# Performance work log

Hardware: AMD Instinct MI355X
Metric: run time of the kernel (lower is better)

Reference implementation:

```python
import jax, jax.numpy as jnp
import numpy as np

D_EMBED = 2048
N_HEAD = 16
HEAD_DIM = D_EMBED // N_HEAD
B, S = 4, 2048


def setup_inputs() -> dict:
    key = jax.random.key(0)
    ks = jax.random.split(key, 6)
    s = 0.02
    x = jax.random.normal(ks[0], (B, S, D_EMBED), dtype=jnp.float32)
    attention_mask = jnp.ones((B, S), dtype=bool)
    Wq = jax.random.normal(ks[1], (D_EMBED, D_EMBED), dtype=jnp.float32) * s
    Wk = jax.random.normal(ks[2], (D_EMBED, D_EMBED), dtype=jnp.float32) * s
    Wv = jax.random.normal(ks[3], (D_EMBED, D_EMBED), dtype=jnp.float32) * s
    Wo = jax.random.normal(ks[4], (D_EMBED, D_EMBED), dtype=jnp.float32) * s
    bq = jnp.zeros((D_EMBED,), jnp.float32)
    bk = jnp.zeros((D_EMBED,), jnp.float32)
    bv = jnp.zeros((D_EMBED,), jnp.float32)
    bo = jnp.zeros((D_EMBED,), jnp.float32)
    return {"x": x, "attention_mask": attention_mask,
            "Wq": Wq, "bq": bq, "Wk": Wk, "bk": bk,
            "Wv": Wv, "bv": bv, "Wo": Wo, "bo": bo}


def reference(x, attention_mask, Wq, bq, Wk, bk, Wv, bv, Wo, bo):
    bsz, seq_len, _ = x.shape

    def split_heads(t):  # [B,S,D] -> [B,H,S,hd]
        return t.reshape(bsz, seq_len, N_HEAD, HEAD_DIM).transpose(0, 2, 1, 3)

    q = split_heads(x @ Wq + bq)
    k = split_heads(x @ Wk + bk)
    v = split_heads(x @ Wv + bv)

    scale = 1.0 / np.sqrt(HEAD_DIM).astype(np.float32)
    scores = jnp.einsum('bhqd,bhkd->bhqk', q, k) * scale  # [B,H,S,S]

    # causal (past_len = 0, query_len = total_len = S) combined with key padding mask
    causal = jnp.tril(jnp.ones((seq_len, seq_len), dtype=bool))  # [S,S]
    mask = causal[None, None, :, :] & attention_mask[:, None, None, :]
    neg = jnp.finfo(scores.dtype).min
    scores = jnp.where(mask, scores, neg)

    att = jax.nn.softmax(scores, axis=-1)  # dropout p=0.0 -> identity
    out = jnp.einsum('bhqk,bhkd->bhqd', att, v)
    out = out.transpose(0, 2, 1, 3).reshape(bsz, seq_len, D_EMBED)
    return out @ Wo + bo
```

## Files before the change

### kernel.cpp

```cpp
#include <hip/hip_runtime.h>
#include <cstdint>
#include <cstddef>


#define D_EMBED 2048
#define NHEAD   16
#define HDIM    128
#define BATCH   4
#define SEQ     2048
#define MROWS   (BATCH*SEQ)

typedef __attribute__((ext_vector_type(8))) short bf16x8;
typedef __attribute__((ext_vector_type(4))) float f32x4;

__device__ __forceinline__ short f2bf(float f) {
  union { float f; uint32_t u; } v; v.f = f;
  uint32_t r = v.u + 0x7fffu + ((v.u >> 16) & 1u);
  return (short)(r >> 16);
}

__device__ __forceinline__ void async_copy16(void* lds, const void* gmem) {
  __builtin_amdgcn_global_load_lds(
      (__attribute__((address_space(1))) void*)gmem,
      (__attribute__((address_space(3))) void*)lds, 16, 0, 0);
}

__global__ __launch_bounds__(256) void cvt_x(const float* __restrict__ x,
                                             short* __restrict__ xb) {
  int i = blockIdx.x * 256 + threadIdx.x;
  float4 v = reinterpret_cast<const float4*>(x)[i];
  short4 o;
  o.x = f2bf(v.x); o.y = f2bf(v.y); o.z = f2bf(v.z); o.w = f2bf(v.w);
  reinterpret_cast<short4*>(xb)[i] = o;
}

struct TransArgs { const float* src[4]; short* dst[4]; };

__global__ __launch_bounds__(256) void transpose_w(TransArgs ta) {
  const int z = blockIdx.z;
  const float* W = ta.src[z];
  short* Wt = ta.dst[z];
  __shared__ float tile[32][33];
  int bx = blockIdx.x * 32, by = blockIdx.y * 32;
  int tx = threadIdx.x & 31, ty = threadIdx.x >> 5;
#pragma unroll
  for (int r = ty; r < 32; r += 8)
    tile[r][tx] = W[(size_t)(by + r) * D_EMBED + bx + tx];
  __syncthreads();
#pragma unroll
  for (int r = ty; r < 32; r += 8)
    Wt[(size_t)(bx + r) * D_EMBED + by + tx] = f2bf(tile[tx][r]);
}

struct GemmArgs {
  const short* A;
  const short* Bt[3];
  const float* bias[3];
  void*        out[3];
  float        scale[3];
  int          mode[3];
};

__global__ __launch_bounds__(512, 2) void gemm256(GemmArgs ga) {
  const int z = blockIdx.z;
  const short* __restrict__ A  = ga.A;
  const short* __restrict__ Bt = ga.Bt[z];

  const int lin  = blockIdx.y * 8 + blockIdx.x;
  const int wg   = (lin & 7) * 32 + (lin >> 3);
  const int col0 = (wg & 7) * 256;
  const int row0 = (wg >> 3) * 256;

  __shared__ __align__(16) short As[2][2][2][64 * 64];
  __shared__ __align__(16) short Bs[2][2][128 * 64];

  const int tid  = threadIdx.x;
  const int lane = tid & 63, w = tid >> 6;
  const int lr   = lane & 15, quad = lane >> 4;
  const int wm   = w >> 2, wn = w & 3;
  const int lr8  = lane >> 3;
  const int srccol = ((lane & 7) ^ ((lane >> 3) & 7)) * 8;
  const int csw = (quad ^ (lr & 7)) * 8;

  bf16x8 av[4][2], bva[2][2], bvb[2][2];
  f32x4 acc[8][4] = {};

#define STAGE_A(buf, Mh, kk) do {                                              \
    _Pragma("unroll")                                                          \
    for (int j = 0; j < 2; ++j)                                                \
      async_copy16(&As[buf][Mh][j][w * 512],                                   \
          A + (size_t)(row0 + j * 128 + (Mh) * 64 + w * 8 + lr8) * D_EMBED +   \
              (kk) + srccol);                                                  \
  } while (0)

#define STAGE_B(buf, Nh, kk) do {                                              \
    _Pragma("unroll")                                                          \
    for (int j = 0; j < 2; ++j) {                                              \
      int fr_ = j * 64 + w * 8 + lr8;                                          \
      async_copy16(&Bs[buf][Nh][(j * 64 + w * 8) * 64],                        \
          Bt + (size_t)(col0 + (fr_ >> 5) * 64 + (Nh) * 32 + (fr_ & 31)) *     \
                  D_EMBED + (kk) + srccol);                                    \
    }                                                                          \
  } while (0)

#define LOAD_A(buf, Mh) do {                                                   \
    _Pragma("unroll")                                                          \
    for (int t = 0; t < 4; ++t) {                                              \
      const short* ap_ = &As[buf][Mh][wm][(t * 16 + lr) * 64];                 \
      av[t][0] = *reinterpret_cast<const bf16x8*>(ap_ + csw);                  \
      av[t][1] = *reinterpret_cast<const bf16x8*>(ap_ + (csw ^ 32));           \
    }                                                                          \
  } while (0)

#define LOAD_B(buf, Nh, dst) do {                                              \
    _Pragma("unroll")                                                          \
    for (int u = 0; u < 2; ++u) {                                              \
      const short* bp_ = &Bs[buf][Nh][(wn * 32 + u * 16 + lr) * 64];           \
      dst[u][0] = *reinterpret_cast<const bf16x8*>(bp_ + csw);                 \
      dst[u][1] = *reinterpret_cast<const bf16x8*>(bp_ + (csw ^ 32));          \
    }                                                                          \
  } while (0)

#define MFMA_Q(Mh, Nh, bv) do {                                                \
    _Pragma("unroll")                                                          \
    for (int ks = 0; ks < 2; ++ks)                                             \
      _Pragma("unroll")                                                        \
      for (int t = 0; t < 4; ++t)                                              \
        _Pragma("unroll")                                                      \
        for (int u = 0; u < 2; ++u)                                            \
          acc[(Mh) * 4 + t][(Nh) * 2 + u] =                                    \
              __builtin_amdgcn_mfma_f32_16x16x32_bf16(                         \
                  av[t][ks], bv[u][ks], acc[(Mh) * 4 + t][(Nh) * 2 + u],       \
                  0, 0, 0);                                                    \
  } while (0)

#define PHASE(Mh, Nh, bv) do {                                                 \
    __builtin_amdgcn_s_setprio(1);                                             \
    MFMA_Q(Mh, Nh, bv);                                                        \
    __builtin_amdgcn_s_setprio(0);                                             \
    __builtin_amdgcn_s_barrier();                                              \
  } while (0)

  STAGE_A(0, 0, 0);  STAGE_B(0, 0, 0);  STAGE_B(0, 1, 0);  STAGE_A(0, 1, 0);
  STAGE_A(1, 0, 64); STAGE_B(1, 0, 64); STAGE_B(1, 1, 64); STAGE_A(1, 1, 64);
  asm volatile("s_waitcnt vmcnt(0)" ::: "memory");
  __builtin_amdgcn_s_barrier();
  LOAD_B(0, 0, bva);

#pragma unroll 1
  for (int it = 0; it < 16; ++it) {
    const int kc = it * 128;
    LOAD_A(0, 0); LOAD_B(0, 1, bvb);
    PHASE(0, 0, bva);
    STAGE_A(0, 0, kc + 128); STAGE_B(0, 0, kc + 128);
    PHASE(0, 1, bvb);
    LOAD_A(0, 1);
    STAGE_B(0, 1, kc + 128);
    PHASE(1, 1, bvb);
    LOAD_B(1, 0, bvb);
    STAGE_A(0, 1, kc + 128);
    asm volatile("s_waitcnt vmcnt(4)" ::: "memory");
    PHASE(1, 0, bva);
    LOAD_A(1, 0); LOAD_B(1, 1, bva);
    PHASE(0, 0, bvb);
    STAGE_B(1, 0, kc + 192); STAGE_A(1, 0, kc + 192);
    PHASE(0, 1, bva);
    LOAD_A(1, 1);
    STAGE_B(1, 1, kc + 192);
    PHASE(1, 1, bva);
    LOAD_B(0, 0, bva);
    STAGE_A(1, 1, kc + 192);
    asm volatile("s_waitcnt vmcnt(4)" ::: "memory");
    PHASE(1, 0, bvb);
  }
  asm volatile("s_waitcnt vmcnt(0)" ::: "memory");

#undef STAGE_A
#undef STAGE_B
#undef LOAD_A
#undef LOAD_B
#undef MFMA_Q
#undef PHASE

  const float* __restrict__ bias = ga.bias[z];
  const int mode = ga.mode[z];
  const float scl = ga.scale[z];
  if (mode != 2) {
#pragma unroll
    for (int mi = 0; mi < 8; ++mi)
#pragma unroll
      for (int ni = 0; ni < 4; ++ni) {
        int n = col0 + wn * 64 + ni * 16 + lr;
        float bias_n = bias[n];
#pragma unroll
        for (int i = 0; i < 4; ++i) {
          int m = row0 + wm * 128 + mi * 16 + quad * 4 + i;
          float v = (acc[mi][ni][i] + bias_n) * scl;
          if (mode == 0) ((short*)ga.out[z])[(size_t)m * D_EMBED + n] = f2bf(v);
          else           ((float*)ga.out[z])[(size_t)m * D_EMBED + n] = v;
        }
      }
  } else {
    short* Vt = (short*)ga.out[z];
#pragma unroll
    for (int ni = 0; ni < 4; ++ni) {
      int n = col0 + wn * 64 + ni * 16 + lr;
      int h = n >> 7, dd = n & (HDIM - 1);
      float bias_n = bias[n];
#pragma unroll
      for (int mi = 0; mi < 8; ++mi)
#pragma unroll
        for (int i = 0; i < 4; ++i) {
          int m = row0 + wm * 128 + mi * 16 + quad * 4 + i;
          int b = m >> 11, t = m & (SEQ - 1);
          Vt[(size_t)((b * NHEAD + h) * HDIM + dd) * SEQ + t] = f2bf(acc[mi][ni][i] + bias_n);
        }
    }
  }
}

#define QK_ONE(Kp, qf, sc)                                                      \
  {                                                                             \
    _Pragma("unroll")                                                           \
    for (int nt = 0; nt < 4; ++nt) sc[nt] = (f32x4){0.f, 0.f, 0.f, 0.f};        \
    __builtin_amdgcn_s_setprio(1);                                              \
    _Pragma("unroll")                                                           \
    for (int nt = 0; nt < 4; ++nt)                                              \
      _Pragma("unroll")                                                         \
      for (int ks = 0; ks < 4; ++ks) {                                          \
        bf16x8 kf = *reinterpret_cast<const bf16x8*>(                           \
            &(Kp)[(nt * 16 + lr) * 128 + (((ks * 4 + quad) ^ lr) * 8)]);        \
        sc[nt] = __builtin_amdgcn_mfma_f32_16x16x32_bf16(qf[ks], kf, sc[nt], 0, 0, 0); \
      }                                                                         \
    __builtin_amdgcn_s_setprio(0);                                              \
  }

#define SM_ONE(sc, l_i, qrow, diag, t0)                                         \
  {                                                                             \
    if (diag) {                                                                 \
      _Pragma("unroll")                                                         \
      for (int nt = 0; nt < 4; ++nt) {                                          \
        int t = (t0) + nt * 16 + lr;                                            \
        _Pragma("unroll")                                                       \
        for (int i = 0; i < 4; ++i)                                             \
          if (t > (qrow) + quad * 4 + i) sc[nt][i] = -1e30f;                    \
      }                                                                         \
    }                                                                           \
    _Pragma("unroll")                                                           \
    for (int nt = 0; nt < 4; ++nt)                                              \
      _Pragma("unroll")                                                         \
      for (int i = 0; i < 4; ++i) {                                             \
        float p = exp2f(sc[nt][i]);                                             \
        l_i[i] += p;                                                            \
        Pls[wave][(quad * 4 + i) * 72 + nt * 16 + lr] = f2bf(p);                \
      }                                                                         \
  }

#define PV_ONE(Vp, o)                                                           \
  {                                                                             \
    __builtin_amdgcn_s_setprio(1);                                              \
    _Pragma("unroll")                                                           \
    for (int n2 = 0; n2 < 8; ++n2)                                              \
      _Pragma("unroll")                                                         \
      for (int k2 = 0; k2 < 2; ++k2) {                                          \
        bf16x8 pf = *reinterpret_cast<const bf16x8*>(                           \
            &Pls[wave][lr * 72 + k2 * 32 + quad * 8]);                          \
        bf16x8 vf = *reinterpret_cast<const bf16x8*>(                           \
            &(Vp)[(n2 * 16 + lr) * 64 + (((k2 * 4 + quad) ^ (lr & 7)) * 8)]);   \
        o[n2] = __builtin_amdgcn_mfma_f32_16x16x32_bf16(pf, vf, o[n2], 0, 0, 0);\
      }                                                                         \
    __builtin_amdgcn_s_setprio(0);                                              \
  }

#define FINALIZE_STRIP(o, l_i, qrow)                                            \
  {                                                                             \
    _Pragma("unroll")                                                           \
    for (int off = 1; off < 16; off <<= 1)                                      \
      _Pragma("unroll")                                                         \
      for (int i = 0; i < 4; ++i) l_i[i] += __shfl_xor(l_i[i], off);            \
    float inv_l[4];                                                             \
    _Pragma("unroll")                                                           \
    for (int i = 0; i < 4; ++i) inv_l[i] = 1.0f / l_i[i];                       \
    short* obase = O + (size_t)(b * SEQ + (qrow)) * D_EMBED + h * HDIM;         \
    _Pragma("unroll")                                                           \
    for (int n2 = 0; n2 < 8; ++n2)                                              \
      _Pragma("unroll")                                                         \
      for (int i = 0; i < 4; ++i)                                               \
        obase[(size_t)(quad * 4 + i) * D_EMBED + n2 * 16 + lr] =                \
            f2bf(o[n2][i] * inv_l[i]);                                          \
  }

#define STAGE_K(cb, tbase)                                                      \
  {                                                                             \
    _Pragma("unroll")                                                           \
    for (int s = 0; s < 4; ++s) {                                               \
      int r0 = wave * 16 + s * 4;                                               \
      int r  = r0 + krow;                                                       \
      int cg = (kcg_base ^ ((s * 4 + krow) & 15)) * 8;                          \
      async_copy16(&Kls[cb][r0 * 128],                                          \
                   Kbase + (size_t)((tbase) + r) * D_EMBED + cg);               \
    }                                                                           \
  }

#define STAGE_V(cb, tbase)                                                      \
  {                                                                             \
    _Pragma("unroll")                                                           \
    for (int s = 0; s < 4; ++s) {                                               \
      int r0 = wave * 32 + s * 8;                                               \
      int r  = r0 + vrow;                                                       \
      async_copy16(&Vls[cb][r0 * 64],                                           \
                   Vtbase + (size_t)r * SEQ + (tbase) + vcg);                   \
    }                                                                           \
  }

__global__ __launch_bounds__(256, 2) void flash_attn(const short* __restrict__ Q,
                                                     const short* __restrict__ K,
                                                     const short* __restrict__ Vt,
                                                     short* __restrict__ O) {
  __shared__ short Kls[2][64 * 128];
  __shared__ short Vls[2][128 * 64];
  __shared__ short Pls[4][16 * 72];

  const int lane = threadIdx.x & 63, wave = threadIdx.x >> 6;
  const int lr = lane & 15, quad = lane >> 4;
  const int b = blockIdx.z, h = blockIdx.y;
  const int qb_lo = blockIdx.x;
  const int qb_hi = 31 - qb_lo;
  const int qrow_lo = qb_lo * 64 + wave * 16;
  const int qrow_hi = qb_hi * 64 + wave * 16;

  const int krow = lane >> 4;
  const int kcg_base = lane & 15;
  const int vrow = lane >> 3;
  const int vcg = ((lane & 7) ^ (lane >> 3)) * 8;

  bf16x8 qf_lo[4], qf_hi[4];
  {
    const short* qp0 = Q + (size_t)(b * SEQ + qrow_lo + lr) * D_EMBED + h * HDIM;
    const short* qp1 = Q + (size_t)(b * SEQ + qrow_hi + lr) * D_EMBED + h * HDIM;
#pragma unroll
    for (int ks = 0; ks < 4; ++ks) {
      qf_lo[ks] = *reinterpret_cast<const bf16x8*>(qp0 + ks * 32 + quad * 8);
      qf_hi[ks] = *reinterpret_cast<const bf16x8*>(qp1 + ks * 32 + quad * 8);
    }
  }

  f32x4 o_lo[8] = {}, o_hi[8] = {};
  float l_lo[4] = {}, l_hi[4] = {};

  const short* Kbase  = K + (size_t)b * SEQ * D_EMBED + h * HDIM;
  const short* Vtbase = Vt + (size_t)((b * NHEAD + h) * HDIM) * SEQ;

  STAGE_K(0, 0); STAGE_V(0, 0); STAGE_K(1, 64);
  asm volatile("s_waitcnt vmcnt(0)" ::: "memory");
  __builtin_amdgcn_s_barrier();

  f32x4 sc_hi[4], sc_lo[4];
  QK_ONE(&Kls[0][0], qf_hi, sc_hi);
  QK_ONE(&Kls[0][0], qf_lo, sc_lo);
  __builtin_amdgcn_s_barrier();

  for (int tt = 0; tt <= qb_hi; ++tt) {
    const int t0 = tt * 64;
    const int nxt = (tt + 1) & 1;
    if (tt + 2 <= qb_hi) STAGE_K(tt & 1, t0 + 128);
    if (tt + 1 <= qb_hi) STAGE_V(nxt, t0 + 64);

    SM_ONE(sc_hi, l_hi, qrow_hi, tt == qb_hi, t0);
    if (tt + 1 <= qb_hi) QK_ONE(&Kls[nxt][0], qf_hi, sc_hi);
    PV_ONE(&Vls[tt & 1][0], o_hi);

    if (tt <= qb_lo) {
      SM_ONE(sc_lo, l_lo, qrow_lo, tt == qb_lo, t0);
      if (tt + 1 <= qb_lo) QK_ONE(&Kls[nxt][0], qf_lo, sc_lo);
      PV_ONE(&Vls[tt & 1][0], o_lo);
    }

    __syncthreads();
  }

  FINALIZE_STRIP(o_hi, l_hi, qrow_hi);
  FINALIZE_STRIP(o_lo, l_lo, qrow_lo);
}

extern "C" void kernel_launch(void* const* d_in, const int* in_sizes, int n_in,
                              void* d_out, int out_size, void* d_ws, size_t ws_size,
                              hipStream_t stream) {
  const float* x  = (const float*)d_in[0];
  const float* Wq = (const float*)d_in[2];
  const float* bq = (const float*)d_in[3];
  const float* Wk = (const float*)d_in[4];
  const float* bk = (const float*)d_in[5];
  const float* Wv = (const float*)d_in[6];
  const float* bv = (const float*)d_in[7];
  const float* Wo = (const float*)d_in[8];
  const float* bo = (const float*)d_in[9];

  char* ws = (char*)d_ws;
  const size_t MB32 = (size_t)MROWS * D_EMBED * 2;
  const size_t WSZ  = (size_t)D_EMBED * D_EMBED * 2;
  short* Xb   = (short*)(ws);
  short* Wqt  = (short*)(ws + MB32);
  short* Wkt  = (short*)(ws + MB32 + WSZ);
  short* Wvt  = (short*)(ws + MB32 + 2 * WSZ);
  short* Wot  = (short*)(ws + MB32 + 3 * WSZ);
  short* Qb   = (short*)(ws + 2 * MB32);
  short* Kb   = (short*)(ws + 3 * MB32);
  short* Vtb  = (short*)(ws + 4 * MB32);
  short* attn = Xb;

  const float scale2 = 0.08838834764831845f * 1.4426950408889634f;

  cvt_x<<<(MROWS * D_EMBED) / 4 / 256, 256, 0, stream>>>(x, Xb);

  TransArgs ta{{Wq, Wk, Wv, Wo}, {Wqt, Wkt, Wvt, Wot}};
  transpose_w<<<dim3(64, 64, 4), 256, 0, stream>>>(ta);

  GemmArgs ga;
  ga.A = Xb;
  ga.Bt[0] = Wqt; ga.Bt[1] = Wkt; ga.Bt[2] = Wvt;
  ga.bias[0] = bq; ga.bias[1] = bk; ga.bias[2] = bv;
  ga.out[0] = Qb; ga.out[1] = Kb; ga.out[2] = Vtb;
  ga.scale[0] = scale2; ga.scale[1] = 1.f; ga.scale[2] = 1.f;
  ga.mode[0] = 0; ga.mode[1] = 0; ga.mode[2] = 2;
  gemm256<<<dim3(D_EMBED / 256, MROWS / 256, 3), 512, 0, stream>>>(ga);

  flash_attn<<<dim3(16, NHEAD, BATCH), 256, 0, stream>>>(Qb, Kb, Vtb, attn);

  GemmArgs gb;
  gb.A = attn;
  gb.Bt[0] = Wot; gb.Bt[1] = Wot; gb.Bt[2] = Wot;
  gb.bias[0] = bo; gb.bias[1] = bo; gb.bias[2] = bo;
  gb.out[0] = d_out; gb.out[1] = d_out; gb.out[2] = d_out;
  gb.scale[0] = 1.f; gb.scale[1] = 1.f; gb.scale[2] = 1.f;
  gb.mode[0] = 1; gb.mode[1] = 1; gb.mode[2] = 1;
  gemm256<<<dim3(D_EMBED / 256, MROWS / 256, 1), 512, 0, stream>>>(gb);
}
```

Baseline: 577.7 us.

## Split fused QKV GEMM into separate launches and remap flash-attn blocks per XCD

The single z-batched QKV GEMM launch becomes three separate launches, each with scalar arguments, so one weight matrix's tiles stay resident in L2 per launch instead of three interleaved. Flash attention now uses a 1D grid of 1024 blocks whose index is remapped so blocks sharing the same batch/head land on the same XCD (lin & 7), improving K/V L2 reuse. The cost is extra kernel launch overhead and possible tail effects between the now-serialized GEMMs.

Measured after the change: 540.5 us. -6.4%, faster.

```diff
diff --git a/kernel.cpp b/kernel.cpp
--- a/kernel.cpp
+++ b/kernel.cpp
@@ -54,17 +54,16 @@
 
 struct GemmArgs {
   const short* A;
-  const short* Bt[3];
-  const float* bias[3];
-  void*        out[3];
-  float        scale[3];
-  int          mode[3];
+  const short* Bt;
+  const float* bias;
+  void*        out;
+  float        scale;
+  int          mode;
 };
 
 __global__ __launch_bounds__(512, 2) void gemm256(GemmArgs ga) {
-  const int z = blockIdx.z;
   const short* __restrict__ A  = ga.A;
-  const short* __restrict__ Bt = ga.Bt[z];
+  const short* __restrict__ Bt = ga.Bt;
 
   const int lin  = blockIdx.y * 8 + blockIdx.x;
   const int wg   = (lin & 7) * 32 + (lin >> 3);
@@ -182,9 +181,9 @@
 #undef MFMA_Q
 #undef PHASE
 
-  const float* __restrict__ bias = ga.bias[z];
-  const int mode = ga.mode[z];
-  const float scl = ga.scale[z];
+  const float* __restrict__ bias = ga.bias;
+  const int mode = ga.mode;
+  const float scl = ga.scale;
   if (mode != 2) {
 #pragma unroll
     for (int mi = 0; mi < 8; ++mi)
@@ -196,12 +195,12 @@
         for (int i = 0; i < 4; ++i) {
           int m = row0 + wm * 128 + mi * 16 + quad * 4 + i;
           float v = (acc[mi][ni][i] + bias_n) * scl;
-          if (mode == 0) ((short*)ga.out[z])[(size_t)m * D_EMBED + n] = f2bf(v);
-          else           ((float*)ga.out[z])[(size_t)m * D_EMBED + n] = v;
+          if (mode == 0) ((short*)ga.out)[(size_t)m * D_EMBED + n] = f2bf(v);
+          else           ((float*)ga.out)[(size_t)m * D_EMBED + n] = v;
         }
       }
   } else {
-    short* Vt = (short*)ga.out[z];
+    short* Vt = (short*)ga.out;
 #pragma unroll
     for (int ni = 0; ni < 4; ++ni) {
       int n = col0 + wn * 64 + ni * 16 + lr;
@@ -323,9 +322,14 @@
 
   const int lane = threadIdx.x & 63, wave = threadIdx.x >> 6;
   const int lr = lane & 15, quad = lane >> 4;
-  const int b = blockIdx.z, h = blockIdx.y;
-  const int qb_lo = blockIdx.x;
-  const int qb_hi = 31 - qb_lo;
+
+  const int lin  = blockIdx.x;
+  const int xcd  = lin & 7, slot = lin >> 3;
+  const int g    = ((slot >> 4) << 3) + xcd;
+  const int s0   = slot & 15;
+  const int h    = g & 15, b = g >> 4;
+  const int qb_lo = s0;
+  const int qb_hi = 31 - s0;
   const int qrow_lo = qb_lo * 64 + wave * 16;
   const int qrow_hi = qb_hi * 64 + wave * 16;
 
@@ -416,23 +420,17 @@
   TransArgs ta{{Wq, Wk, Wv, Wo}, {Wqt, Wkt, Wvt, Wot}};
   transpose_w<<<dim3(64, 64, 4), 256, 0, stream>>>(ta);
 
-  GemmArgs ga;
-  ga.A = Xb;
-  ga.Bt[0] = Wqt; ga.Bt[1] = Wkt; ga.Bt[2] = Wvt;
-  ga.bias[0] = bq; ga.bias[1] = bk; ga.bias[2] = bv;
-  ga.out[0] = Qb; ga.out[1] = Kb; ga.out[2] = Vtb;
-  ga.scale[0] = scale2; ga.scale[1] = 1.f; ga.scale[2] = 1.f;
-  ga.mode[0] = 0; ga.mode[1] = 0; ga.mode[2] = 2;
-  gemm256<<<dim3(D_EMBED / 256, MROWS / 256, 3), 512, 0, stream>>>(ga);
-
-  flash_attn<<<dim3(16, NHEAD, BATCH), 256, 0, stream>>>(Qb, Kb, Vtb, attn);
-
-  GemmArgs gb;
-  gb.A = attn;
-  gb.Bt[0] = Wot; gb.Bt[1] = Wot; gb.Bt[2] = Wot;
-  gb.bias[0] = bo; gb.bias[1] = bo; gb.bias[2] = bo;
-  gb.out[0] = d_out; gb.out[1] = d_out; gb.out[2] = d_out;
-  gb.scale[0] = 1.f; gb.scale[1] = 1.f; gb.scale[2] = 1.f;
-  gb.mode[0] = 1; gb.mode[1] = 1; gb.mode[2] = 1;
-  gemm256<<<dim3(D_EMBED / 256, MROWS / 256, 1), 512, 0, stream>>>(gb);
-}
+  const dim3 ggrid(D_EMBED / 256, MROWS / 256, 1);
+
+  GemmArgs gq{Xb, Wqt, bq, Qb,  scale2, 0};
+  gemm256<<<ggrid, 512, 0, stream>>>(gq);
+  GemmArgs gk{Xb, Wkt, bk, Kb,  1.f,    0};
+  gemm256<<<ggrid, 512, 0, stream>>>(gk);
+  GemmArgs gv{Xb, Wvt, bv, Vtb, 1.f,    2};
+  gemm256<<<ggrid, 512, 0, stream>>>(gv);
+
+  flash_attn<<<dim3(1024, 1, 1), 256, 0, stream>>>(Qb, Kb, Vtb, attn);
+
+  GemmArgs go{attn, Wot, bo, d_out, 1.f, 1};
+  gemm256<<<ggrid, 512, 0, stream>>>(go);
+}
```
